# Performance work log

Measured on AMD Instinct MI355X. Metric: run time of the kernel, lower is better.

Reference implementation:

```python
import jax, jax.numpy as jnp
import numpy as np

HEAD_DIM = 32
NUM_HEADS = 12
GP_NUM = 48
TOPK = 96


def setup_inputs() -> dict:
    key = jax.random.key(0)
    k0, k1, k2, k3 = jax.random.split(key, 4)
    B, H, W, C = 2, 40, 40, 384
    x = jax.random.normal(k0, (B, H, W, C), dtype=jnp.float32)
    w_qkv = jax.random.normal(k1, (3 * NUM_HEADS * HEAD_DIM, C), dtype=jnp.float32) * 0.05
    w_gp = jax.random.normal(k2, (GP_NUM, C), dtype=jnp.float32) * 0.05
    w_proj = jax.random.normal(k3, (C, NUM_HEADS * HEAD_DIM), dtype=jnp.float32) * 0.05
    return {"x": x, "w_qkv": w_qkv, "w_gp": w_gp, "w_proj": w_proj}


def _forward(x, w_qkv, w_gp, w_proj):
    B, H, W, C = x.shape
    N = H * W
    h, d, G, K = NUM_HEADS, HEAD_DIM, GP_NUM, TOPK
    scale = d ** -0.5
    qkv = (x.reshape(B, N, C) @ w_qkv.T).reshape(B, N, 3, h, d)
    qkv = qkv.transpose(2, 0, 3, 1, 4)  # [3,B,h,N,d]
    q, k, v = qkv[0], qkv[1], qkv[2]
    # dense attention [B,h,N,N]
    attn = jax.nn.softmax(jnp.einsum('bhnd,bhmd->bhnm', q, k) * scale, axis=-1)
    # query -> group routing (top-1 one-hot)
    gp = w_gp.reshape(h, G, d)
    group_logits = jnp.einsum('bhnd,hgd->bhng', q, gp)
    gidx = jnp.argmax(group_logits, axis=-1)  # [B,h,N]
    gw = jax.nn.one_hot(gidx, G, dtype=q.dtype)  # [B,h,N,G]
    # group-mean queries
    q_mean = jnp.einsum('bhng,bhnd->bhgd', gw, q)
    num_per_group = gw.sum(axis=2)[..., None]  # [B,h,G,1]
    q_mean = q_mean / jnp.clip(num_per_group, 1e-8)
    # group -> key routing (top-K scatter mask)
    qmw = jnp.einsum('bhgd,bhmd->bhgm', q_mean, k)  # [B,h,G,N]
    _, idx = jax.lax.top_k(qmw, K)  # [B,h,G,K]
    idx_flat = idx.reshape(-1, K)
    rows = jnp.arange(idx_flat.shape[0])[:, None]
    mask = jnp.zeros((idx_flat.shape[0], N), dtype=q.dtype).at[rows, idx_flat].set(1.0)
    mask = mask.reshape(qmw.shape)  # [B,h,G,N]
    # compose query->group and group->key masks, renormalize
    final = jnp.einsum('bhng,bhgm->bhnm', gw, mask)
    attn = attn * final
    attn = attn / jnp.clip(attn.sum(axis=-1, keepdims=True), 1e-8)
    out = jnp.einsum('bhnm,bhmd->bhnd', attn, v)
    out = out.transpose(0, 2, 1, 3).reshape(B, H, W, h * d)
    return out @ w_proj.T


def reference(x, w_qkv, w_gp, w_proj):
    return _forward(x, w_qkv, w_gp, w_proj)
```

## Files before the change

### kernel.cpp

```cpp
#include <hip/hip_runtime.h>
#include <math.h>

#define NH 12
#define HD 32
#define GN 48
#define TK 96
#define NB 2
#define NN 1600
#define CC 384
#define BHN (NB*NH)
#define QKV_COLS (3*NH*HD)
#define NQ (BHN*NN)
#define KP 36
#define LP 68

template<int MODE>
__global__ __launch_bounds__(256)
void gemm_tile(const float* __restrict__ A, const float* __restrict__ B,
               float* __restrict__ o0, float* __restrict__ o1, float* __restrict__ o2,
               int M, int N, int K)
{
    __shared__ float As[16][LP];
    __shared__ float Bs[16][LP];
    const int tid = threadIdx.x;
    const int tx = tid & 15, ty = tid >> 4;
    const int m0 = blockIdx.y * 64, n0 = blockIdx.x * 64;
    const int lr = tid >> 2;
    const int lc = (tid & 3) * 4;
    float acc[4][4] = {};

    for (int k0 = 0; k0 < K; k0 += 16) {
        float4 av = *(const float4*)&A[(m0 + lr) * K + k0 + lc];
        float4 bv = *(const float4*)&B[(n0 + lr) * K + k0 + lc];
        __syncthreads();
        As[lc+0][lr] = av.x; As[lc+1][lr] = av.y; As[lc+2][lr] = av.z; As[lc+3][lr] = av.w;
        Bs[lc+0][lr] = bv.x; Bs[lc+1][lr] = bv.y; Bs[lc+2][lr] = bv.z; Bs[lc+3][lr] = bv.w;
        __syncthreads();
        #pragma unroll
        for (int kk = 0; kk < 16; ++kk) {
            float4 a4 = *(const float4*)&As[kk][ty*4];
            float4 b4 = *(const float4*)&Bs[kk][tx*4];
            float a[4] = {a4.x, a4.y, a4.z, a4.w};
            float b[4] = {b4.x, b4.y, b4.z, b4.w};
            #pragma unroll
            for (int i = 0; i < 4; ++i)
                #pragma unroll
                for (int j = 0; j < 4; ++j)
                    acc[i][j] = fmaf(a[i], b[j], acc[i][j]);
        }
    }

    if (MODE == 0) {
        #pragma unroll
        for (int i = 0; i < 4; ++i) {
            int row = m0 + ty*4 + i;
            int b  = row / NN;
            int nn = row - b * NN;
            #pragma unroll
            for (int j = 0; j < 4; ++j) {
                int col = n0 + tx*4 + j;
                int which = col / CC;
                int rem = col - which * CC;
                int hh = rem >> 5, dd = rem & 31;
                float* dst = (which == 0) ? o0 : (which == 1) ? o1 : o2;
                dst[((b*NH + hh)*NN + nn)*HD + dd] = acc[i][j];
            }
        }
    } else {
        #pragma unroll
        for (int i = 0; i < 4; ++i) {
            int row = m0 + ty*4 + i;
            float4 st = make_float4(acc[i][0], acc[i][1], acc[i][2], acc[i][3]);
            *(float4*)&o0[row * N + n0 + tx*4] = st;
        }
    }
}

__global__ __launch_bounds__(256)
void group_route(const float* __restrict__ q, const float* __restrict__ wgp,
                 int* __restrict__ gidx)
{
    int t = blockIdx.x * 256 + threadIdx.x;
    int bh = t / NN;
    int hh = bh % NH;
    const float* qp = q + t * HD;
    float qr[HD];
    #pragma unroll
    for (int i = 0; i < HD; i += 4) {
        float4 x = *(const float4*)&qp[i];
        qr[i] = x.x; qr[i+1] = x.y; qr[i+2] = x.z; qr[i+3] = x.w;
    }
    float best = -INFINITY; int bg = 0;
    for (int g = 0; g < GN; ++g) {
        const float* gp = wgp + hh*GN*HD + g*HD;
        float s = 0.f;
        #pragma unroll
        for (int i = 0; i < HD; i += 4) {
            float4 w = *(const float4*)&gp[i];
            s += qr[i]*w.x + qr[i+1]*w.y + qr[i+2]*w.z + qr[i+3]*w.w;
        }
        if (s > best) { best = s; bg = g; }
    }
    gidx[t] = bg;
}

__global__ __launch_bounds__(256)
void qmean_all2(const float* __restrict__ q, const int* __restrict__ gidx,
                float* __restrict__ qmean, int* __restrict__ qperm,
                int* __restrict__ qoff, int* __restrict__ qcnt)
{
    __shared__ float part[8][HD];
    __shared__ int   cnts[8];
    __shared__ int   off_s, pos_s;
    const int bid = blockIdx.x;
    const int g = bid % GN, bh = bid / GN;
    const int tid = threadIdx.x;
    const int s = tid >> 5, dd = tid & 31;

    const int* __restrict__ gx = gidx + bh*NN;
    const float* __restrict__ qb = q + bh*NN*HD;

    if (tid == 0) { off_s = 0; pos_s = 0; }

    const int base = s * 200;
    float p = 0.f; int c = 0;
    #pragma unroll 2
    for (int n0 = 0; n0 < 200; n0 += 4) {
        int4 g4 = *(const int4*)&gx[base + n0];
        float v0 = qb[(base+n0+0)*HD + dd];
        float v1 = qb[(base+n0+1)*HD + dd];
        float v2 = qb[(base+n0+2)*HD + dd];
        float v3 = qb[(base+n0+3)*HD + dd];
        if (g4.x == g) { p += v0; c++; }
        if (g4.y == g) { p += v1; c++; }
        if (g4.z == g) { p += v2; c++; }
        if (g4.w == g) { p += v3; c++; }
    }
    part[s][dd] = p;
    if (dd == 0) cnts[s] = c;
    __syncthreads();

    if (tid < HD) {
        float sum = 0.f; int ct = 0;
        #pragma unroll
        for (int ss = 0; ss < 8; ++ss) { sum += part[ss][tid]; ct += cnts[ss]; }
        qmean[bid*HD + tid] = ct ? sum / (float)ct : 0.f;
    }

    int mo = 0;
    for (int n = tid; n < NN; n += 256) mo += (gx[n] < g);
    atomicAdd(&off_s, mo);
    __syncthreads();
    for (int n = tid; n < NN; n += 256) {
        if (gx[n] == g) {
            int pp = atomicAdd(&pos_s, 1);
            qperm[bh*NN + off_s + pp] = n;
        }
    }
    __syncthreads();
    if (tid == 0) { qoff[bid] = off_s; qcnt[bid] = pos_s; }
}

__global__ __launch_bounds__(256)
void score_all(const float* __restrict__ qmean, const float* __restrict__ k,
               float* __restrict__ scores)
{
    __shared__ float Qs[GN][HD];
    const int bh = blockIdx.y;
    const int tid = threadIdx.x;
    const int n = blockIdx.x*256 + tid;
    for (int i = tid; i < GN*HD; i += 256)
        ((float*)Qs)[i] = qmean[bh*GN*HD + i];
    __syncthreads();
    if (n >= NN) return;
    const float* __restrict__ kp = k + (bh*NN + n)*HD;
    float4 kr[8];
    #pragma unroll
    for (int c = 0; c < 8; ++c) kr[c] = *(const float4*)&kp[c*4];
    for (int g = 0; g < GN; ++g) {
        float s = 0.f;
        #pragma unroll
        for (int c = 0; c < 8; ++c) {
            float4 qv = *(const float4*)&Qs[g][c*4];
            s += kr[c].x*qv.x + kr[c].y*qv.y + kr[c].z*qv.z + kr[c].w*qv.w;
        }
        scores[(bh*GN + g)*NN + n] = s;
    }
}

__global__ __launch_bounds__(256)
void topk_radix(const float* __restrict__ scores, int* __restrict__ topk)
{
    __shared__ unsigned keysL[4][NN];
    __shared__ unsigned histL[4][256];
    const int tid = threadIdx.x;
    const int w = tid >> 6, lane = tid & 63;
    const int gid = blockIdx.x*4 + w;
    const float* __restrict__ row = scores + gid*NN;
    unsigned* keys = keysL[w];
    unsigned* hist = histL[w];

    #pragma unroll
    for (int i = 0; i < 25; ++i) {
        int m = lane + 64*i;
        unsigned u = __float_as_uint(row[m]);
        u = (u & 0x80000000u) ? ~u : (u | 0x80000000u);
        keys[m] = u;
    }

    unsigned prefix = 0, r = TK;
    #pragma unroll
    for (int pass = 0; pass < 4; ++pass) {
        const int shift = 24 - 8*pass;
        #pragma unroll
        for (int j = 0; j < 4; ++j) hist[lane*4 + j] = 0;
        #pragma unroll
        for (int i = 0; i < 25; ++i) {
            unsigned u = keys[lane + 64*i];
            bool match = (pass == 0) || ((u >> (shift+8)) == (prefix >> (shift+8)));
            if (match) atomicAdd(&hist[(u >> shift) & 255u], 1u);
        }
        uint4 h = *(const uint4*)&hist[lane*4];
        unsigned s3 = h.w, s2 = h.z + s3, s1 = h.y + s2, s0 = h.x + s1;
        unsigned I = s0;
        #pragma unroll
        for (int off = 1; off < 64; off <<= 1) {
            unsigned t = __shfl_down(I, off);
            if (lane + off < 64) I += t;
        }
        unsigned E = I - s0;
        unsigned sf[5] = {E+s0, E+s1, E+s2, E+s3, E};
        int bj = -1; unsigned subc = 0;
        #pragma unroll
        for (int j = 0; j < 4; ++j)
            if (sf[j] >= r && sf[j+1] < r) { bj = j; subc = sf[j+1]; }
        unsigned long long mask = __ballot(bj >= 0);
        int src = __ffsll(mask) - 1;
        int bstar = __shfl(lane*4 + bj, src);
        unsigned sub = (unsigned)__shfl((int)subc, src);
        prefix |= ((unsigned)bstar) << shift;
        r -= sub;
    }
    const unsigned P = prefix;

    int* tko = topk + gid*TK;
    int base = 0;
    #pragma unroll
    for (int i = 0; i < 25; ++i) {
        int m = lane + 64*i;
        bool gt = (keys[m] > P);
        unsigned long long mask = __ballot(gt);
        if (gt) tko[base + __popcll(mask & ((1ull << lane) - 1ull))] = m;
        base += (int)__popcll(mask);
    }
    #pragma unroll
    for (int i = 0; i < 25; ++i) {
        int m = lane + 64*i;
        bool eq = (keys[m] == P);
        unsigned long long mask = __ballot(eq);
        if (eq) {
            int pos = base + (int)__popcll(mask & ((1ull << lane) - 1ull));
            if (pos < TK) tko[pos] = m;
        }
        base += (int)__popcll(mask);
    }
}

__global__ __launch_bounds__(256)
void sparse_attn8(const float* __restrict__ q, const float* __restrict__ k,
                  const float* __restrict__ v, const int* __restrict__ topk,
                  const int* __restrict__ qperm, const int* __restrict__ qoff,
                  const int* __restrict__ qcnt, float* __restrict__ out)
{
    __shared__ float Ks[TK*KP];
    __shared__ float Vs[TK*HD];
    __shared__ float Ps[32][104];

    const int sub = blockIdx.x & 1;
    const int bid = blockIdx.x >> 1;
    const int bh = bid / GN;
    const int nq = qcnt[bid];
    if (nq <= sub*32) return;
    const int off = qoff[bid];
    const int tid = threadIdx.x;

    const int* __restrict__ tk = topk + bid*TK;
    const float* __restrict__ kb = k + bh*NN*HD;
    const float* __restrict__ vb = v + bh*NN*HD;

    for (int idx = tid; idx < TK*8; idx += 256) {
        int row = idx >> 3, ch = idx & 7;
        int r = tk[row];
        *(float4*)&Ks[row*KP + ch*4] = *(const float4*)&kb[r*HD + ch*4];
        ((float4*)Vs)[idx] = *(const float4*)&vb[r*HD + ch*4];
    }
    __syncthreads();

    const float scale = 0.17677669529663687f;
    const int qs = tid >> 3;
    const int dl = tid & 7;
    const int b = bh / NH, hh = bh - b*NH;
    const float* __restrict__ qbase = q + bh*NN*HD;
    const int* __restrict__ qlist = qperm + bh*NN + off;

    for (int it0 = sub*32; it0 < nq; it0 += 64) {
        const int qi = it0 + qs;
        const bool act = (qi < nq);
        const int nn = qlist[act ? qi : nq-1];

        float4 qr[8];
        #pragma unroll
        for (int c = 0; c < 8; ++c) qr[c] = *(const float4*)&qbase[nn*HD + c*4];

        #pragma unroll 2
        for (int t = 0; t < 12; ++t) {
            const int j = t*8 + dl;
            float s0 = 0.f, s1 = 0.f, s2 = 0.f, s3 = 0.f;
            #pragma unroll
            for (int c = 0; c < 8; ++c) {
                float4 w = *(const float4*)&Ks[j*KP + c*4];
                s0 = fmaf(qr[c].x, w.x, s0);
                s1 = fmaf(qr[c].y, w.y, s1);
                s2 = fmaf(qr[c].z, w.z, s2);
                s3 = fmaf(qr[c].w, w.w, s3);
            }
            Ps[qs][j] = ((s0 + s1) + (s2 + s3)) * scale;
        }

        float raw[12];
        #pragma unroll
        for (int t = 0; t < 12; ++t) raw[t] = Ps[qs][t*8 + dl];
        float m = -INFINITY;
        #pragma unroll
        for (int t = 0; t < 12; ++t) m = fmaxf(m, raw[t]);
        #pragma unroll
        for (int o = 1; o < 8; o <<= 1) m = fmaxf(m, __shfl_xor(m, o));
        float l = 0.f;
        #pragma unroll
        for (int t = 0; t < 12; ++t) l += __expf(raw[t] - m);
        #pragma unroll
        for (int o = 1; o < 8; o <<= 1) l += __shfl_xor(l, o);
        const float inv = 1.0f / l;
        #pragma unroll
        for (int t = 0; t < 12; ++t) Ps[qs][t*8 + dl] = __expf(raw[t] - m) * inv;

        float a0 = 0.f, a1 = 0.f, a2 = 0.f, a3 = 0.f;
        #pragma unroll 4
        for (int j = 0; j < TK; ++j) {
            const float p = Ps[qs][j];
            float4 vv = *(const float4*)&Vs[j*HD + dl*4];
            a0 = fmaf(p, vv.x, a0);
            a1 = fmaf(p, vv.y, a1);
            a2 = fmaf(p, vv.z, a2);
            a3 = fmaf(p, vv.w, a3);
        }

        if (act) {
            float* op = out + (b*NN + nn)*CC + hh*HD + dl*4;
            *(float4*)op = make_float4(a0, a1, a2, a3);
        }
    }
}

extern "C" void kernel_launch(void* const* d_in, const int* in_sizes, int n_in,
                              void* d_out, int out_size, void* d_ws, size_t ws_size,
                              hipStream_t stream)
{
    const float* x      = (const float*)d_in[0];
    const float* w_qkv  = (const float*)d_in[1];
    const float* w_gp   = (const float*)d_in[2];
    const float* w_proj = (const float*)d_in[3];
    float* out = (float*)d_out;

    float* ws = (float*)d_ws;
    float* q        = ws;
    float* kk       = ws + 1228800;
    float* vv       = ws + 2457600;
    float* attn_out = ws + 3686400;
    float* scores   = ws + 4915200;
    float* qmean    = ws + 6758400;
    int*   iws      = (int*)(ws + 6795264);
    int*   gidx     = iws;
    int*   topk     = iws + 38400;
    int*   qperm    = iws + 38400 + 110592;
    int*   qoff     = iws + 38400 + 110592 + 38400;
    int*   qcnt     = qoff + 1152;

    gemm_tile<0><<<dim3(QKV_COLS/64, (NB*NN)/64), 256, 0, stream>>>(
        x, w_qkv, q, kk, vv, NB*NN, QKV_COLS, CC);

    group_route<<<NQ/256, 256, 0, stream>>>(q, w_gp, gidx);

    qmean_all2<<<BHN*GN, 256, 0, stream>>>(q, gidx, qmean, qperm, qoff, qcnt);

    score_all<<<dim3(7, BHN), 256, 0, stream>>>(qmean, kk, scores);

    topk_radix<<<(BHN*GN)/4, 256, 0, stream>>>(scores, topk);

    sparse_attn8<<<BHN*GN*2, 256, 0, stream>>>(q, kk, vv, topk, qperm, qoff, qcnt, attn_out);

    gemm_tile<1><<<dim3(CC/64, (NB*NN)/64), 256, 0, stream>>>(
        attn_out, w_proj, out, nullptr, nullptr, NB*NN, CC, CC);
}
```

Baseline: 249.6 us.

## Use single-wavefront GEMM blocks with 8x8 register tiles and vector stores

```diff
diff --git a/kernel.cpp b/kernel.cpp
--- a/kernel.cpp
+++ b/kernel.cpp
@@ -15,7 +15,7 @@
 #define LP 68
 
 template<int MODE>
-__global__ __launch_bounds__(256)
+__global__ __launch_bounds__(64)
 void gemm_tile(const float* __restrict__ A, const float* __restrict__ B,
                float* __restrict__ o0, float* __restrict__ o1, float* __restrict__ o2,
                int M, int N, int K)
@@ -23,55 +23,71 @@
     __shared__ float As[16][LP];
     __shared__ float Bs[16][LP];
     const int tid = threadIdx.x;
-    const int tx = tid & 15, ty = tid >> 4;
+    const int tx = tid & 7;
+    const int ty = tid >> 3;
     const int m0 = blockIdx.y * 64, n0 = blockIdx.x * 64;
     const int lr = tid >> 2;
     const int lc = (tid & 3) * 4;
-    float acc[4][4] = {};
+    float acc[8][8] = {};
 
     for (int k0 = 0; k0 < K; k0 += 16) {
-        float4 av = *(const float4*)&A[(m0 + lr) * K + k0 + lc];
-        float4 bv = *(const float4*)&B[(n0 + lr) * K + k0 + lc];
-        __syncthreads();
-        As[lc+0][lr] = av.x; As[lc+1][lr] = av.y; As[lc+2][lr] = av.z; As[lc+3][lr] = av.w;
-        Bs[lc+0][lr] = bv.x; Bs[lc+1][lr] = bv.y; Bs[lc+2][lr] = bv.z; Bs[lc+3][lr] = bv.w;
-        __syncthreads();
-        #pragma unroll
+        float4 av[4], bv[4];
+        #pragma unroll
+        for (int r = 0; r < 4; ++r) {
+            av[r] = *(const float4*)&A[(m0 + lr + 16*r) * K + k0 + lc];
+            bv[r] = *(const float4*)&B[(n0 + lr + 16*r) * K + k0 + lc];
+        }
+        #pragma unroll
+        for (int r = 0; r < 4; ++r) {
+            As[lc+0][lr+16*r] = av[r].x; As[lc+1][lr+16*r] = av[r].y;
+            As[lc+2][lr+16*r] = av[r].z; As[lc+3][lr+16*r] = av[r].w;
+            Bs[lc+0][lr+16*r] = bv[r].x; Bs[lc+1][lr+16*r] = bv[r].y;
+            Bs[lc+2][lr+16*r] = bv[r].z; Bs[lc+3][lr+16*r] = bv[r].w;
+        }
+        #pragma unroll 2
         for (int kk = 0; kk < 16; ++kk) {
-            float4 a4 = *(const float4*)&As[kk][ty*4];
-            float4 b4 = *(const float4*)&Bs[kk][tx*4];
-            float a[4] = {a4.x, a4.y, a4.z, a4.w};
-            float b[4] = {b4.x, b4.y, b4.z, b4.w};
+            float4 aa0 = *(const float4*)&As[kk][ty*8];
+            float4 aa1 = *(const float4*)&As[kk][ty*8+4];
+            float4 bb0 = *(const float4*)&Bs[kk][tx*8];
+            float4 bb1 = *(const float4*)&Bs[kk][tx*8+4];
+            float a[8] = {aa0.x,aa0.y,aa0.z,aa0.w,aa1.x,aa1.y,aa1.z,aa1.w};
+            float b[8] = {bb0.x,bb0.y,bb0.z,bb0.w,bb1.x,bb1.y,bb1.z,bb1.w};
             #pragma unroll
-            for (int i = 0; i < 4; ++i)
+            for (int i = 0; i < 8; ++i)
                 #pragma unroll
-                for (int j = 0; j < 4; ++j)
+                for (int j = 0; j < 8; ++j)
                     acc[i][j] = fmaf(a[i], b[j], acc[i][j]);
         }
     }
 
     if (MODE == 0) {
         #pragma unroll
-        for (int i = 0; i < 4; ++i) {
-            int row = m0 + ty*4 + i;
+        for (int i = 0; i < 8; ++i) {
+            int row = m0 + ty*8 + i;
             int b  = row / NN;
             int nn = row - b * NN;
             #pragma unroll
-            for (int j = 0; j < 4; ++j) {
-                int col = n0 + tx*4 + j;
+            for (int jg = 0; jg < 2; ++jg) {
+                int col = n0 + tx*8 + jg*4;
                 int which = col / CC;
                 int rem = col - which * CC;
                 int hh = rem >> 5, dd = rem & 31;
                 float* dst = (which == 0) ? o0 : (which == 1) ? o1 : o2;
-                dst[((b*NH + hh)*NN + nn)*HD + dd] = acc[i][j];
+                *(float4*)&dst[((b*NH + hh)*NN + nn)*HD + dd] =
+                    make_float4(acc[i][jg*4+0], acc[i][jg*4+1],
+                                acc[i][jg*4+2], acc[i][jg*4+3]);
             }
         }
     } else {
         #pragma unroll
-        for (int i = 0; i < 4; ++i) {
-            int row = m0 + ty*4 + i;
-            float4 st = make_float4(acc[i][0], acc[i][1], acc[i][2], acc[i][3]);
-            *(float4*)&o0[row * N + n0 + tx*4] = st;
+        for (int i = 0; i < 8; ++i) {
+            int row = m0 + ty*8 + i;
+            #pragma unroll
+            for (int jg = 0; jg < 2; ++jg) {
+                *(float4*)&o0[row * N + n0 + tx*8 + jg*4] =
+                    make_float4(acc[i][jg*4+0], acc[i][jg*4+1],
+                                acc[i][jg*4+2], acc[i][jg*4+3]);
+            }
         }
     }
 }
@@ -386,7 +402,7 @@
     int*   qoff     = iws + 38400 + 110592 + 38400;
     int*   qcnt     = qoff + 1152;
 
-    gemm_tile<0><<<dim3(QKV_COLS/64, (NB*NN)/64), 256, 0, stream>>>(
+    gemm_tile<0><<<dim3(QKV_COLS/64, (NB*NN)/64), 64, 0, stream>>>(
         x, w_qkv, q, kk, vv, NB*NN, QKV_COLS, CC);
 
     group_route<<<NQ/256, 256, 0, stream>>>(q, w_gp, gidx);
@@ -399,6 +415,6 @@
 
     sparse_attn8<<<BHN*GN*2, 256, 0, stream>>>(q, kk, vv, topk, qperm, qoff, qcnt, attn_out);
 
-    gemm_tile<1><<<dim3(CC/64, (NB*NN)/64), 256, 0, stream>>>(
+    gemm_tile<1><<<dim3(CC/64, (NB*NN)/64), 64, 0, stream>>>(
         attn_out, w_proj, out, nullptr, nullptr, NB*NN, CC, CC);
 }
```

Measured after the change: 290.9 us. +16.6%, slower.
